# Optimization experiments

Measured on AMD Instinct MI355X. Metric: run time of the kernel, lower is better.

Reference implementation:

```python
import jax, jax.numpy as jnp
import numpy as np

EPS = 1e-5
SLOPE = 0.2


def _conv3d(x, w, stride):
    # x: [B, Cin, D, H, W], w: [Cout, Cin, 3, 3, 3]
    return jax.lax.conv_general_dilated(
        x, w, window_strides=(stride, stride, stride),
        padding=[(1, 1), (1, 1), (1, 1)],
        dimension_numbers=("NCDHW", "OIDHW", "NCDHW"))


def _layernorm_c(y, g, b):
    # LayerNorm over the channel (feature) dim, matching nn.LayerNorm(C) on [N, C]
    mu = jnp.mean(y, axis=1, keepdims=True)
    var = jnp.mean((y - mu) ** 2, axis=1, keepdims=True)
    yn = (y - mu) * jax.lax.rsqrt(var + EPS)
    return yn * g[None, :, None, None, None] + b[None, :, None, None, None]


def _leaky(y):
    return jnp.where(y > 0, y, SLOPE * y)


def _block(x, m, w, g, b, stride):
    # x already zero at inactive sites, so dense conv == sparse gather-scatter conv
    y = _conv3d(x, w, stride)
    if stride > 1:
        # strided SparseConv3d: output active iff any input in 3x3x3 window active
        ones_k = jnp.ones((1, 1, 3, 3, 3), x.dtype)
        m = (_conv3d(m, ones_k, stride) > 0).astype(x.dtype)
    y = _leaky(_layernorm_c(y, g, b))
    return y * m, m


def setup_inputs() -> dict:
    key = jax.random.key(0)
    ks = jax.random.split(key, 16)
    B, D = 2, 64
    x = jax.random.normal(ks[0], (B, 3, D, D, D), jnp.float32)
    mask = jax.random.randint(ks[1], (B, D, D, D), 0, 2) > 0
    chans = [(3, 64), (64, 128), (128, 256), (256, 512)]
    inp = {"x": x, "mask": mask}
    for i, (ci, co) in enumerate(chans):
        inp[f"w{i+1}"] = jax.random.normal(ks[2 + 3 * i], (co, ci, 3, 3, 3), jnp.float32) * 0.05
        inp[f"g{i+1}"] = jnp.ones((co,), jnp.float32)
        inp[f"b{i+1}"] = jnp.zeros((co,), jnp.float32)
    return inp


def reference(x, mask, w1, g1, b1, w2, g2, b2, w3, g3, b3, w4, g4, b4):
    m = mask.astype(x.dtype)[:, None]          # [B,1,D,H,W]
    x = x * m                                  # zero inactive sites
    # SubMConv3d: active set unchanged (stride 1)
    y, m = _block(x, m, w1, g1, b1, 1)
    y, m = _block(y, m, w2, g2, b2, 2)
    y, m = _block(y, m, w3, g3, b3, 2)
    y, m = _block(y, m, w4, g4, b4, 2)
    # .dense() fills inactive sites with 0 (already the case), then amax over D,H,W
    return jnp.max(y, axis=(2, 3, 4))          # [B, 512]
```

## Files before the change

kernel.cpp:

```cpp
#include <hip/hip_runtime.h>
#include <hip/hip_bf16.h>
#include <stdint.h>

#define EPS 1e-5f
#define SLOPE 0.2f

typedef __attribute__((ext_vector_type(8))) short short8;
typedef __attribute__((ext_vector_type(4))) float f32x4;

static __device__ inline ushort f2bf(float f) {
  __hip_bfloat16 h = __float2bfloat16(f);
  return *reinterpret_cast<ushort*>(&h);
}

static __device__ inline short8 u4_to_s8(uint a, uint b, uint c, uint d) {
  union { uint4 u; short8 s; } cv;
  cv.u.x = a; cv.u.y = b; cv.u.z = c; cv.u.w = d;
  return cv.s;
}

__global__ void mask_detect_k(const uint8_t* __restrict__ raw, int nbytes,
                              unsigned* __restrict__ flag) {
  unsigned local = 0;
  for (int i = blockIdx.x * blockDim.x + threadIdx.x; i < nbytes;
       i += gridDim.x * blockDim.x)
    if (i & 3) local |= raw[i];
  if (local) atomicOr(flag, 1u);
}

__global__ void xclm_k(const float* __restrict__ x, const uint8_t* __restrict__ raw,
                       const unsigned* __restrict__ flag,
                       uint8_t* __restrict__ m1, ushort* __restrict__ xcl) {
  int id = blockIdx.x * blockDim.x + threadIdx.x;
  if (id >= 2 * 262144) return;
  uint8_t v;
  if (*flag) {
    v = raw[id];
  } else {
    size_t j = 4 * (size_t)id;
    v = (uint8_t)(raw[j] | raw[j + 1] | raw[j + 2] | raw[j + 3]);
  }
  v = v ? 1 : 0;
  m1[id] = v;
  float mk = (float)v;
  int b  = id >> 18;
  int sp = id & 262143;
  size_t base = (size_t)b * 3 * 262144 + sp;
  float x0 = x[base] * mk;
  float x1 = x[base + 262144] * mk;
  float x2 = x[base + 2 * 262144] * mk;
  uint2 u;
  u.x = ((uint)f2bf(x1) << 16) | (uint)f2bf(x0);
  u.y = (uint)f2bf(x2);
  *reinterpret_cast<uint2*>(xcl + (size_t)id * 4) = u;
}

__global__ void mask_down_k(const uint8_t* __restrict__ mi,
                            uint8_t* __restrict__ mo, int DIN) {
  int W = DIN >> 1;
  int id = blockIdx.x * blockDim.x + threadIdx.x;
  int total = 2 * W * W * W;
  if (id >= total) return;
  int xo = id % W; int t = id / W;
  int yo = t % W;  t /= W;
  int zo = t % W;  int b = t / W;
  int any = 0;
  for (int dz = 0; dz < 3; ++dz) {
    int z = 2 * zo + dz - 1; if (z < 0 || z >= DIN) continue;
    for (int dy = 0; dy < 3; ++dy) {
      int y = 2 * yo + dy - 1; if (y < 0 || y >= DIN) continue;
      for (int dx = 0; dx < 3; ++dx) {
        int x = 2 * xo + dx - 1; if (x < 0 || x >= DIN) continue;
        any |= mi[(((size_t)b * DIN + z) * DIN + y) * DIN + x];
      }
    }
  }
  mo[id] = any ? 1 : 0;
}

__global__ void wprep_k(const float* __restrict__ w1, const float* __restrict__ w2,
                        const float* __restrict__ w3, const float* __restrict__ w4,
                        ushort* __restrict__ wb1, ushort* __restrict__ wb2,
                        ushort* __restrict__ wb3, ushort* __restrict__ wb4) {
  int id = blockIdx.x * blockDim.x + threadIdx.x;
  if (id < 8192) {
    int k = id & 127, c = id >> 7;
    int tap = k >> 2, ci = k & 3;
    float v = (tap < 27 && ci < 3) ? w1[c * 81 + ci * 27 + tap] : 0.f;
    wb1[id] = f2bf(v);
    return;
  }
  id -= 8192;
  if (id < 128 * 1728) {
    int kn = id % 1728, c = id / 1728;
    int off = kn >> 6, ci = kn & 63;
    wb2[(size_t)c * 1728 + kn] = f2bf(w2[(size_t)c * 1728 + ci * 27 + off]);
    return;
  }
  id -= 128 * 1728;
  if (id < 256 * 3456) {
    int kn = id % 3456, c = id / 3456;
    int off = kn >> 7, ci = kn & 127;
    wb3[(size_t)c * 3456 + kn] = f2bf(w3[(size_t)c * 3456 + ci * 27 + off]);
    return;
  }
  id -= 256 * 3456;
  if (id < 512 * 6912) {
    int kn = id % 6912, c = id / 6912;
    int off = kn >> 8, ci = kn & 255;
    wb4[(size_t)c * 6912 + kn] = f2bf(w4[(size_t)c * 6912 + ci * 27 + off]);
  }
}

__global__ __launch_bounds__(256) void conv1_gemm(
    const ushort* __restrict__ xcl,
    const ushort* __restrict__ wb1,
    const float* __restrict__ gamma,
    const float* __restrict__ beta,
    const uint8_t* __restrict__ msk,
    ushort* __restrict__ out,
    const ushort* __restrict__ zpage)
{
  const int t    = threadIdx.x;
  const int lane = t & 63;
  const int wave = t >> 6;
  int bid = blockIdx.x;
  bid = (bid & 7) * 512 + (bid >> 3);
  const int n0 = bid * 128;
  const int wn = wave * 32;

  __shared__ short As[2][64 * 64];
  __shared__ short Bs[2][128 * 64];

  const int nl   = t & 127;
  const int kchi = t >> 7;
  const int ng = n0 + nl;
  const int bx = ng & 63, by = (ng >> 6) & 63, bz = (ng >> 12) & 63;
  const long basevox = (long)ng * 4;
  const bool okx0 = bx > 0, okx2 = bx < 63;
  const bool oky0 = by > 0, oky2 = by < 63;
  const bool okz0 = bz > 0, okz2 = bz < 63;
  int bswz[4];
#pragma unroll
  for (int j = 0; j < 4; ++j) {
    int kc = kchi + 2 * j;
    bswz[j] = nl * 64 + ((kc ^ (nl & 7)) << 3);
  }
  int aswz[2];
  const ushort* aptr[2];
#pragma unroll
  for (int j = 0; j < 2; ++j) {
    int q = t + 256 * j, ml = q >> 3, kc = q & 7;
    aswz[j] = ml * 64 + ((kc ^ (ml & 7)) << 3);
    aptr[j] = wb1 + ml * 128 + kc * 8;
  }

  short8 ar[2], br[4];

  auto LOADK = [&](int kb) {
#pragma unroll
    for (int j = 0; j < 2; ++j)
      ar[j] = *reinterpret_cast<const short8*>(aptr[j] + kb * 64);
#pragma unroll
    for (int j = 0; j < 4; ++j) {
      int tp0 = kb * 16 + (kchi + 2 * j) * 2;
      uint wrd[4];
#pragma unroll
      for (int h = 0; h < 2; ++h) {
        int tp = tp0 + h;
        int dz = tp / 9, rr = tp - dz * 9;
        int dy = rr / 3, dx = rr - dy * 3;
        bool ok = (tp < 27)
               && (dz != 0 || okz0) && (dz != 2 || okz2)
               && (dy != 0 || oky0) && (dy != 2 || oky2)
               && (dx != 0 || okx0) && (dx != 2 || okx2);
        long toff = (long)(((dz - 1) * 4096 + (dy - 1) * 64 + (dx - 1)) * 4);
        const ushort* p = ok ? (xcl + basevox + toff) : zpage;
        uint2 v = *reinterpret_cast<const uint2*>(p);
        wrd[2 * h] = v.x; wrd[2 * h + 1] = v.y;
      }
      br[j] = u4_to_s8(wrd[0], wrd[1], wrd[2], wrd[3]);
    }
  };

  auto WRITEK = [&](int buf) {
#pragma unroll
    for (int j = 0; j < 2; ++j)
      *reinterpret_cast<short8*>(&As[buf][aswz[j]]) = ar[j];
#pragma unroll
    for (int j = 0; j < 4; ++j)
      *reinterpret_cast<short8*>(&Bs[buf][bswz[j]]) = br[j];
  };

  f32x4 acc[4][2];
#pragma unroll
  for (int i = 0; i < 4; ++i)
#pragma unroll
    for (int j = 0; j < 2; ++j) acc[i][j] = (f32x4)(0.f);

  auto COMPUTE = [&](int buf) {
    short8 afr[4][2], bfr[2][2];
#pragma unroll
    for (int mf = 0; mf < 4; ++mf)
#pragma unroll
      for (int kh = 0; kh < 2; ++kh) {
        int row  = mf * 16 + (lane & 15);
        int slot = (lane >> 4) + kh * 4;
        afr[mf][kh] = *reinterpret_cast<const short8*>(
            &As[buf][row * 64 + ((slot ^ (row & 7)) << 3)]);
      }
#pragma unroll
    for (int nf = 0; nf < 2; ++nf)
#pragma unroll
      for (int kh = 0; kh < 2; ++kh) {
        int row  = wn + nf * 16 + (lane & 15);
        int slot = (lane >> 4) + kh * 4;
        bfr[nf][kh] = *reinterpret_cast<const short8*>(
            &Bs[buf][row * 64 + ((slot ^ (row & 7)) << 3)]);
      }
#pragma unroll
    for (int mf = 0; mf < 4; ++mf)
#pragma unroll
      for (int nf = 0; nf < 2; ++nf)
#pragma unroll
        for (int kh = 0; kh < 2; ++kh)
          acc[mf][nf] = __builtin_amdgcn_mfma_f32_16x16x32_bf16(
              afr[mf][kh], bfr[nf][kh], acc[mf][nf], 0, 0, 0);
  };

  LOADK(0);
  WRITEK(0);
  LOADK(1);
  __syncthreads();
  COMPUTE(0);
  WRITEK(1);
  __syncthreads();
  COMPUTE(1);

  float gr[4][4], br_[4][4];
#pragma unroll
  for (int mf = 0; mf < 4; ++mf) {
    int cb = mf * 16 + ((lane >> 4) << 2);
    f32x4 gv = *reinterpret_cast<const f32x4*>(gamma + cb);
    f32x4 bv = *reinterpret_cast<const f32x4*>(beta + cb);
#pragma unroll
    for (int r = 0; r < 4; ++r) { gr[mf][r] = gv[r]; br_[mf][r] = bv[r]; }
  }

#pragma unroll
  for (int nf = 0; nf < 2; ++nf) {
    float s = 0.f, sq = 0.f;
#pragma unroll
    for (int mf = 0; mf < 4; ++mf)
#pragma unroll
      for (int r = 0; r < 4; ++r) {
        float v = acc[mf][nf][r];
        s += v; sq += v * v;
      }
    s  += __shfl_xor(s, 16);  sq += __shfl_xor(sq, 16);
    s  += __shfl_xor(s, 32);  sq += __shfl_xor(sq, 32);
    const float mean = s * (1.f / 64.f);
    const float var  = sq * (1.f / 64.f) - mean * mean;
    const float rstd = rsqrtf(var + EPS);
    const int vox = n0 + wn + nf * 16 + (lane & 15);
    const float mk = msk[vox] ? 1.f : 0.f;
#pragma unroll
    for (int mf = 0; mf < 4; ++mf) {
      uint2 u;
      float r0 = (acc[mf][nf][0] - mean) * rstd * gr[mf][0] + br_[mf][0];
      float r1 = (acc[mf][nf][1] - mean) * rstd * gr[mf][1] + br_[mf][1];
      float r2 = (acc[mf][nf][2] - mean) * rstd * gr[mf][2] + br_[mf][2];
      float r3 = (acc[mf][nf][3] - mean) * rstd * gr[mf][3] + br_[mf][3];
      r0 = (r0 > 0.f ? r0 : SLOPE * r0) * mk;
      r1 = (r1 > 0.f ? r1 : SLOPE * r1) * mk;
      r2 = (r2 > 0.f ? r2 : SLOPE * r2) * mk;
      r3 = (r3 > 0.f ? r3 : SLOPE * r3) * mk;
      u.x = ((uint)f2bf(r1) << 16) | (uint)f2bf(r0);
      u.y = ((uint)f2bf(r3) << 16) | (uint)f2bf(r2);
      *reinterpret_cast<uint2*>(out + (size_t)vox * 64 + mf * 16 +
                                ((lane >> 4) << 2)) = u;
    }
  }
}

__global__ __launch_bounds__(256) void conv2_gemm(
    const ushort* __restrict__ in,
    const ushort* __restrict__ wbf,
    const float* __restrict__ gamma,
    const float* __restrict__ beta,
    const uint8_t* __restrict__ msk,
    ushort* __restrict__ out,
    const ushort* __restrict__ zpage)
{
  constexpr int CIN = 64, DIN = 64, S = 2;
  constexpr int W = 32, K = 1728, NT = 27, LW = 5;

  const int t    = threadIdx.x;
  const int lane = t & 63;
  const int wave = t >> 6;
  int bid = blockIdx.x;
  bid = (bid & 7) * 64 + (bid >> 3);
  const int n0 = bid * 128;

  __shared__ short As[2][128 * 64];
  __shared__ short Bs[2][128 * 64];
  __shared__ float lnS[4][4][16];
  __shared__ float lnQ[4][4][16];

  int zb[4], yb[4], xb[4], kc8[4], swz[4];
  size_t bb[4];
  const ushort* aptr[4];
#pragma unroll
  for (int j = 0; j < 4; ++j) {
    int q  = t + 256 * j;
    int nl = q >> 3, kc = q & 7;
    kc8[j] = kc * 8;
    swz[j] = nl * 64 + ((kc ^ (nl & 7)) << 3);
    int ngv = n0 + nl;
    int xo = ngv & (W - 1), yo = (ngv >> LW) & (W - 1),
        zo = (ngv >> (2 * LW)) & (W - 1), b = ngv >> (3 * LW);
    xb[j] = xo * S; yb[j] = yo * S; zb[j] = zo * S;
    bb[j] = (size_t)b * CIN * DIN * DIN * DIN;
    aptr[j] = wbf + (size_t)nl * K + kc * 8;
  }

  short8 ar[4], br[4];

  auto LOADK = [&](int kb) {
    const int off = kb;
    const int dz = off / 9, rr = off % 9;
    const int dy = rr / 3, dx = rr % 3;
#pragma unroll
    for (int j = 0; j < 4; ++j) {
      ar[j] = *reinterpret_cast<const short8*>(aptr[j] + kb * 64);
      int zin = zb[j] + dz - 1;
      int yin = yb[j] + dy - 1;
      int xin = xb[j] + dx - 1;
      bool ok = ((unsigned)zin < (unsigned)DIN) &&
                ((unsigned)yin < (unsigned)DIN) &&
                ((unsigned)xin < (unsigned)DIN);
      const ushort* p = ok
          ? in + bb[j] + (((size_t)zin * DIN + yin) * DIN + xin) * CIN + kc8[j]
          : zpage;
      br[j] = *reinterpret_cast<const short8*>(p);
    }
  };

  auto WRITEK = [&](int buf) {
#pragma unroll
    for (int j = 0; j < 4; ++j) {
      *reinterpret_cast<short8*>(&As[buf][swz[j]]) = ar[j];
      *reinterpret_cast<short8*>(&Bs[buf][swz[j]]) = br[j];
    }
  };

  f32x4 acc[4][4];
#pragma unroll
  for (int i = 0; i < 4; ++i)
#pragma unroll
    for (int j = 0; j < 4; ++j) acc[i][j] = (f32x4)(0.f);

  const int wm = (wave & 1) * 64;
  const int wn = (wave >> 1) * 64;

  LOADK(0);
  for (int kb = 0; kb < NT; ++kb) {
    const int buf = kb & 1;
    WRITEK(buf);
    if (kb + 1 < NT) LOADK(kb + 1);
    __syncthreads();

    short8 afr[4][2], bfr[4][2];
#pragma unroll
    for (int mf = 0; mf < 4; ++mf)
#pragma unroll
      for (int kh = 0; kh < 2; ++kh) {
        int row  = wm + mf * 16 + (lane & 15);
        int slot = (lane >> 4) + kh * 4;
        afr[mf][kh] = *reinterpret_cast<const short8*>(
            &As[buf][row * 64 + ((slot ^ (row & 7)) << 3)]);
      }
#pragma unroll
    for (int nf = 0; nf < 4; ++nf)
#pragma unroll
      for (int kh = 0; kh < 2; ++kh) {
        int row  = wn + nf * 16 + (lane & 15);
        int slot = (lane >> 4) + kh * 4;
        bfr[nf][kh] = *reinterpret_cast<const short8*>(
            &Bs[buf][row * 64 + ((slot ^ (row & 7)) << 3)]);
      }
#pragma unroll
    for (int mf = 0; mf < 4; ++mf)
#pragma unroll
      for (int nf = 0; nf < 4; ++nf)
#pragma unroll
        for (int kh = 0; kh < 2; ++kh)
          acc[mf][nf] = __builtin_amdgcn_mfma_f32_16x16x32_bf16(
              afr[mf][kh], bfr[nf][kh], acc[mf][nf], 0, 0, 0);
  }

  float sv[4], qv[4];
#pragma unroll
  for (int nf = 0; nf < 4; ++nf) {
    float s = 0.f, sq = 0.f;
#pragma unroll
    for (int mf = 0; mf < 4; ++mf)
#pragma unroll
      for (int r = 0; r < 4; ++r) {
        float v = acc[mf][nf][r];
        s += v; sq += v * v;
      }
    s  += __shfl_xor(s, 16);  sq += __shfl_xor(sq, 16);
    s  += __shfl_xor(s, 32);  sq += __shfl_xor(sq, 32);
    sv[nf] = s; qv[nf] = sq;
  }
  if (lane < 16) {
#pragma unroll
    for (int nf = 0; nf < 4; ++nf) {
      lnS[wave][nf][lane] = sv[nf];
      lnQ[wave][nf][lane] = qv[nf];
    }
  }
  __syncthreads();

  float gr[4][4], br_[4][4];
#pragma unroll
  for (int mf = 0; mf < 4; ++mf) {
    int cb = wm + mf * 16 + ((lane >> 4) << 2);
    f32x4 gv = *reinterpret_cast<const f32x4*>(gamma + cb);
    f32x4 bv = *reinterpret_cast<const f32x4*>(beta + cb);
#pragma unroll
    for (int r = 0; r < 4; ++r) { gr[mf][r] = gv[r]; br_[mf][r] = bv[r]; }
  }

#pragma unroll
  for (int nf = 0; nf < 4; ++nf) {
    const float s  = sv[nf] + lnS[wave ^ 1][nf][lane & 15];
    const float sq = qv[nf] + lnQ[wave ^ 1][nf][lane & 15];
    const float mean = s * (1.f / 128.f);
    const float var  = sq * (1.f / 128.f) - mean * mean;
    const float rstd = rsqrtf(var + EPS);
    const int vox = n0 + wn + nf * 16 + (lane & 15);
    const float mk = msk[vox] ? 1.f : 0.f;
#pragma unroll
    for (int mf = 0; mf < 4; ++mf) {
      uint2 u;
      float r0 = (acc[mf][nf][0] - mean) * rstd * gr[mf][0] + br_[mf][0];
      float r1 = (acc[mf][nf][1] - mean) * rstd * gr[mf][1] + br_[mf][1];
      float r2 = (acc[mf][nf][2] - mean) * rstd * gr[mf][2] + br_[mf][2];
      float r3 = (acc[mf][nf][3] - mean) * rstd * gr[mf][3] + br_[mf][3];
      r0 = (r0 > 0.f ? r0 : SLOPE * r0) * mk;
      r1 = (r1 > 0.f ? r1 : SLOPE * r1) * mk;
      r2 = (r2 > 0.f ? r2 : SLOPE * r2) * mk;
      r3 = (r3 > 0.f ? r3 : SLOPE * r3) * mk;
      u.x = ((uint)f2bf(r1) << 16) | (uint)f2bf(r0);
      u.y = ((uint)f2bf(r3) << 16) | (uint)f2bf(r2);
      *reinterpret_cast<uint2*>(out + (size_t)vox * 128 + wm + mf * 16 +
                                ((lane >> 4) << 2)) = u;
    }
  }
}

template <int CIN, int COUT, int DIN, int S, int L2CIN, int SPLITK>
__global__ __launch_bounds__(256) void conv_gemm(
    const ushort* __restrict__ in,
    const ushort* __restrict__ wbf,
    float* __restrict__ rawout,
    const ushort* __restrict__ zpage)
{
  constexpr int W  = DIN / S;
  constexpr int K  = 27 * CIN;
  constexpr int NT = K / 64;
  constexpr int NTS = NT / SPLITK;
  constexpr int LW = (W == 32) ? 5 : (W == 16) ? 4 : 3;
  constexpr size_t NVOX = (size_t)2 * W * W * W;

  const int t    = threadIdx.x;
  const int lane = t & 63;
  const int wave = t >> 6;
  const int n0   = blockIdx.x * 128;
  const int m0   = blockIdx.y * 128;
  const int kb0  = blockIdx.z * NTS;
  float* rawp = rawout + (size_t)blockIdx.z * NVOX * COUT;

  __shared__ short As[2][128 * 64];
  __shared__ short Bs[2][128 * 64];

  int zb[4], yb[4], xb[4], kc8[4], swz[4];
  size_t bb[4];
  const ushort* aptr[4];
#pragma unroll
  for (int j = 0; j < 4; ++j) {
    int q  = t + 256 * j;
    int nl = q >> 3, kc = q & 7;
    kc8[j] = kc * 8;
    swz[j] = nl * 64 + ((kc ^ (nl & 7)) << 3);
    int ng = n0 + nl;
    int xo = ng & (W - 1), yo = (ng >> LW) & (W - 1),
        zo = (ng >> (2 * LW)) & (W - 1), b = ng >> (3 * LW);
    xb[j] = xo * S; yb[j] = yo * S; zb[j] = zo * S;
    bb[j] = (size_t)b * CIN * DIN * DIN * DIN;
    aptr[j] = wbf + (size_t)(m0 + nl) * K + kc * 8;
  }

  short8 ar[4], br[4];

  auto LOADK = [&](int kb) {
    const int off = (kb * 64) >> L2CIN;
    const int ci0 = (kb * 64) & (CIN - 1);
    const int dz = off / 9, rr = off % 9;
    const int dy = rr / 3, dx = rr % 3;
#pragma unroll
    for (int j = 0; j < 4; ++j) {
      ar[j] = *reinterpret_cast<const short8*>(aptr[j] + kb * 64);
      int zin = zb[j] + dz - 1;
      int yin = yb[j] + dy - 1;
      int xin = xb[j] + dx - 1;
      bool ok = ((unsigned)zin < (unsigned)DIN) &&
                ((unsigned)yin < (unsigned)DIN) &&
                ((unsigned)xin < (unsigned)DIN);
      const ushort* p = ok
          ? in + bb[j] + (((size_t)zin * DIN + yin) * DIN + xin) * CIN + ci0 + kc8[j]
          : zpage;
      br[j] = *reinterpret_cast<const short8*>(p);
    }
  };

  auto WRITEK = [&](int buf) {
#pragma unroll
    for (int j = 0; j < 4; ++j) {
      *reinterpret_cast<short8*>(&As[buf][swz[j]]) = ar[j];
      *reinterpret_cast<short8*>(&Bs[buf][swz[j]]) = br[j];
    }
  };

  f32x4 acc[4][4];
#pragma unroll
  for (int i = 0; i < 4; ++i)
#pragma unroll
    for (int j = 0; j < 4; ++j) acc[i][j] = (f32x4)(0.f);

  const int wm = (wave & 1) * 64;
  const int wn = (wave >> 1) * 64;

  LOADK(kb0);
  for (int kb = kb0; kb < kb0 + NTS; ++kb) {
    const int buf = (kb - kb0) & 1;
    WRITEK(buf);
    if (kb + 1 < kb0 + NTS) LOADK(kb + 1);
    __syncthreads();

    short8 afr[4][2], bfr[4][2];
#pragma unroll
    for (int mf = 0; mf < 4; ++mf)
#pragma unroll
      for (int kh = 0; kh < 2; ++kh) {
        int row  = wm + mf * 16 + (lane & 15);
        int slot = (lane >> 4) + kh * 4;
        afr[mf][kh] = *reinterpret_cast<const short8*>(
            &As[buf][row * 64 + ((slot ^ (row & 7)) << 3)]);
      }
#pragma unroll
    for (int nf = 0; nf < 4; ++nf)
#pragma unroll
      for (int kh = 0; kh < 2; ++kh) {
        int row  = wn + nf * 16 + (lane & 15);
        int slot = (lane >> 4) + kh * 4;
        bfr[nf][kh] = *reinterpret_cast<const short8*>(
            &Bs[buf][row * 64 + ((slot ^ (row & 7)) << 3)]);
      }
#pragma unroll
    for (int mf = 0; mf < 4; ++mf)
#pragma unroll
      for (int nf = 0; nf < 4; ++nf)
#pragma unroll
        for (int kh = 0; kh < 2; ++kh)
          acc[mf][nf] = __builtin_amdgcn_mfma_f32_16x16x32_bf16(
              afr[mf][kh], bfr[nf][kh], acc[mf][nf], 0, 0, 0);
  }

#pragma unroll
  for (int mf = 0; mf < 4; ++mf)
#pragma unroll
    for (int nf = 0; nf < 4; ++nf) {
      int mg = m0 + wm + mf * 16 + ((lane >> 4) << 2);
      int ng = n0 + wn + nf * 16 + (lane & 15);
      *reinterpret_cast<f32x4*>(&rawp[(size_t)ng * COUT + mg]) = acc[mf][nf];
    }
}

template <int C, int NPART, bool BF16OUT>
__global__ __launch_bounds__(256) void ln_mask_k(
    const float* __restrict__ raw,
    const float* __restrict__ gamma,
    const float* __restrict__ beta,
    const uint8_t* __restrict__ msk,
    void* __restrict__ outv, int nvox)
{
  constexpr int E = C / 64;
  const int lane = threadIdx.x & 63;
  const int vox  = blockIdx.x * 4 + (threadIdx.x >> 6);
  if (vox >= nvox) return;

  const size_t stride = (size_t)nvox * C;
  const float* p = raw + (size_t)vox * C;
  float v[E];
  float s = 0.f, sq = 0.f;
#pragma unroll
  for (int e = 0; e < E; ++e) {
    float acc = 0.f;
#pragma unroll
    for (int pt = 0; pt < NPART; ++pt) acc += p[pt * stride + e * 64 + lane];
    v[e] = acc;
    s += acc; sq += acc * acc;
  }
#pragma unroll
  for (int off = 32; off; off >>= 1) {
    s  += __shfl_xor(s, off);
    sq += __shfl_xor(sq, off);
  }
  const float mean = s / (float)C;
  const float var  = sq / (float)C - mean * mean;
  const float rstd = rsqrtf(var + EPS);
  const float mk   = msk[vox] ? 1.f : 0.f;

#pragma unroll
  for (int e = 0; e < E; ++e) {
    int c = e * 64 + lane;
    float r = (v[e] - mean) * rstd * gamma[c] + beta[c];
    r = (r > 0.f ? r : SLOPE * r) * mk;
    if (BF16OUT)
      ((ushort*)outv)[(size_t)vox * C + c] = f2bf(r);
    else
      ((float*)outv)[(size_t)vox * C + c] = r;
  }
}

__global__ __launch_bounds__(256) void ln4max_k(
    const float* __restrict__ raw,
    const float* __restrict__ gamma,
    const float* __restrict__ beta,
    const uint8_t* __restrict__ msk,
    float* __restrict__ pm)
{
  const int t    = threadIdx.x;
  const int lane = t & 63;
  const int wave = t >> 6;
  const int grp  = blockIdx.x;
  const size_t stride = (size_t)1024 * 512;

  float gg[8], bb_[8];
#pragma unroll
  for (int e = 0; e < 8; ++e) {
    int c = e * 64 + lane;
    gg[e] = gamma[c]; bb_[e] = beta[c];
  }

  float vmax[8];
#pragma unroll
  for (int e = 0; e < 8; ++e) vmax[e] = -1e30f;

  for (int it = 0; it < 16; ++it) {
    const int vox = grp * 64 + wave * 16 + it;
    const float* p = raw + (size_t)vox * 512;
    float v[8];
    float s = 0.f, sq = 0.f;
#pragma unroll
    for (int e = 0; e < 8; ++e) {
      float a = 0.f;
#pragma unroll
      for (int pt = 0; pt < 4; ++pt) a += p[pt * stride + e * 64 + lane];
      v[e] = a; s += a; sq += a * a;
    }
#pragma unroll
    for (int off = 32; off; off >>= 1) {
      s  += __shfl_xor(s, off);
      sq += __shfl_xor(sq, off);
    }
    const float mean = s * (1.f / 512.f);
    const float var  = sq * (1.f / 512.f) - mean * mean;
    const float rstd = rsqrtf(var + EPS);
    const float mk   = msk[vox] ? 1.f : 0.f;
#pragma unroll
    for (int e = 0; e < 8; ++e) {
      float r = (v[e] - mean) * rstd * gg[e] + bb_[e];
      r = (r > 0.f ? r : SLOPE * r) * mk;
      vmax[e] = fmaxf(vmax[e], r);
    }
  }

  __shared__ float red[4][512];
#pragma unroll
  for (int e = 0; e < 8; ++e) red[wave][e * 64 + lane] = vmax[e];
  __syncthreads();
  for (int c = t; c < 512; c += 256) {
    float m = fmaxf(fmaxf(red[0][c], red[1][c]), fmaxf(red[2][c], red[3][c]));
    pm[(size_t)grp * 512 + c] = m;
  }
}

__global__ void rmax2_k(const float* __restrict__ pm, float* __restrict__ out) {
  const int b = blockIdx.x;
  const int c = threadIdx.x;
  float m = -1e30f;
  for (int g = 0; g < 8; ++g) m = fmaxf(m, pm[((size_t)b * 8 + g) * 512 + c]);
  out[b * 512 + c] = m;
}

extern "C" void kernel_launch(void* const* d_in, const int* in_sizes, int n_in,
                              void* d_out, int out_size, void* d_ws, size_t ws_size,
                              hipStream_t stream) {
  const float*   x    = (const float*)d_in[0];
  const uint8_t* mraw = (const uint8_t*)d_in[1];
  const float* w1 = (const float*)d_in[2];
  const float* g1 = (const float*)d_in[3];
  const float* b1 = (const float*)d_in[4];
  const float* w2 = (const float*)d_in[5];
  const float* g2 = (const float*)d_in[6];
  const float* b2 = (const float*)d_in[7];
  const float* w3 = (const float*)d_in[8];
  const float* g3 = (const float*)d_in[9];
  const float* b3 = (const float*)d_in[10];
  const float* w4 = (const float*)d_in[11];
  const float* g4 = (const float*)d_in[12];
  const float* b4 = (const float*)d_in[13];
  float* out = (float*)d_out;
  char*  ws  = (char*)d_ws;

  const size_t ZP  = 0;
  const size_t T1  = 256;
  const size_t R3  = 67109120;
  const size_t R4  = R3 + 16777216;
  const size_t T2  = 100663552;
  const size_t T3  = 117440768;
  const size_t PM  = 123732224;
  const size_t XCL = 123764992;
  const size_t WB1 = 127959296;
  const size_t WB2 = 127975680;
  const size_t WB3 = 128418048;
  const size_t WB4 = 130187520;
  const size_t M1  = 137265408;
  const size_t M2  = 137789696;
  const size_t M3  = 137855232;
  const size_t M4  = 137863424;

  unsigned* flag = (unsigned*)(ws + ZP);
  const ushort* zpage = (const ushort*)(ws + ZP + 16);
  ushort* t1  = (ushort*)(ws + T1);
  float*  r3  = (float*)(ws + R3);
  float*  r4  = (float*)(ws + R4);
  ushort* t2  = (ushort*)(ws + T2);
  ushort* t3  = (ushort*)(ws + T3);
  float*  pm  = (float*)(ws + PM);
  ushort* xcl = (ushort*)(ws + XCL);
  ushort* wb1 = (ushort*)(ws + WB1);
  ushort* wb2 = (ushort*)(ws + WB2);
  ushort* wb3 = (ushort*)(ws + WB3);
  ushort* wb4 = (ushort*)(ws + WB4);
  uint8_t* m1 = (uint8_t*)(ws + M1);
  uint8_t* m2 = (uint8_t*)(ws + M2);
  uint8_t* m3 = (uint8_t*)(ws + M3);
  uint8_t* m4 = (uint8_t*)(ws + M4);

  const int NM1 = 2 * 64 * 64 * 64;

  hipMemsetAsync(ws + ZP, 0, 64, stream);
  mask_detect_k<<<256, 256, 0, stream>>>(mraw, NM1, flag);
  xclm_k<<<NM1 / 256, 256, 0, stream>>>(x, mraw, flag, m1, xcl);
  mask_down_k<<<(2 * 32 * 32 * 32 + 255) / 256, 256, 0, stream>>>(m1, m2, 64);
  mask_down_k<<<(2 * 16 * 16 * 16 + 255) / 256, 256, 0, stream>>>(m2, m3, 32);
  mask_down_k<<<(2 * 8 * 8 * 8 + 255) / 256, 256, 0, stream>>>(m3, m4, 16);

  wprep_k<<<18176, 256, 0, stream>>>(w1, w2, w3, w4, wb1, wb2, wb3, wb4);

  conv1_gemm<<<4096, 256, 0, stream>>>(xcl, wb1, g1, b1, m1, t1, zpage);

  conv2_gemm<<<512, 256, 0, stream>>>(t1, wb2, g2, b2, m2, t2, zpage);

  conv_gemm<128, 256, 32, 2, 7, 2><<<dim3(64, 2, 2), 256, 0, stream>>>(t2, wb3, r3, zpage);
  ln_mask_k<256, 2, true><<<8192 / 4, 256, 0, stream>>>(r3, g3, b3, m3, t3, 8192);

  conv_gemm<256, 512, 16, 2, 8, 4><<<dim3(8, 4, 4), 256, 0, stream>>>(t3, wb4, r4, zpage);
  ln4max_k<<<16, 256, 0, stream>>>(r4, g4, b4, m4, pm);

  rmax2_k<<<2, 512, 0, stream>>>(pm, out);

  (void)in_sizes; (void)n_in; (void)out_size; (void)ws_size;
}
```

Before: 203.7 us.

## Pad conv1 input halo and load MFMA fragments directly from global, dropping LDS staging

The first-layer input is written into a zero-padded 66^3 channel-last buffer, so conv1 can gather taps without bounds checks. Conv1 and conv2 no longer stage A and B tiles through shared memory with double buffering and barriers. Each lane loads its MFMA fragments straight from global memory, with boundary taps in conv2 handled by a precomputed bitmask. This removes LDS traffic and __syncthreads, but adds a memset of the padded buffer and more redundant global loads that now rely on cache reuse.

After: 285.7 us. +40.3%, slower.

```diff
diff --git a/kernel.cpp b/kernel.cpp
--- a/kernel.cpp
+++ b/kernel.cpp
@@ -30,7 +30,7 @@
 
 __global__ void xclm_k(const float* __restrict__ x, const uint8_t* __restrict__ raw,
                        const unsigned* __restrict__ flag,
-                       uint8_t* __restrict__ m1, ushort* __restrict__ xcl) {
+                       uint8_t* __restrict__ m1, ushort* __restrict__ xclp) {
   int id = blockIdx.x * blockDim.x + threadIdx.x;
   if (id >= 2 * 262144) return;
   uint8_t v;
@@ -45,6 +45,7 @@
   float mk = (float)v;
   int b  = id >> 18;
   int sp = id & 262143;
+  int xx = sp & 63, yy = (sp >> 6) & 63, zz = sp >> 12;
   size_t base = (size_t)b * 3 * 262144 + sp;
   float x0 = x[base] * mk;
   float x1 = x[base + 262144] * mk;
@@ -52,7 +53,8 @@
   uint2 u;
   u.x = ((uint)f2bf(x1) << 16) | (uint)f2bf(x0);
   u.y = (uint)f2bf(x2);
-  *reinterpret_cast<uint2*>(xcl + (size_t)id * 4) = u;
+  size_t pidx = ((((size_t)(b * 66 + zz + 1)) * 66 + (yy + 1)) * 66 + (xx + 1)) * 4;
+  *reinterpret_cast<uint2*>(xclp + pidx) = u;
 }
 
 __global__ void mask_down_k(const uint8_t* __restrict__ mi,
@@ -113,84 +115,58 @@
 }
 
 __global__ __launch_bounds__(256) void conv1_gemm(
-    const ushort* __restrict__ xcl,
+    const ushort* __restrict__ xclp,
     const ushort* __restrict__ wb1,
     const float* __restrict__ gamma,
     const float* __restrict__ beta,
     const uint8_t* __restrict__ msk,
-    ushort* __restrict__ out,
-    const ushort* __restrict__ zpage)
+    ushort* __restrict__ out)
 {
   const int t    = threadIdx.x;
   const int lane = t & 63;
   const int wave = t >> 6;
+  const int c8   = lane >> 4;
   int bid = blockIdx.x;
   bid = (bid & 7) * 512 + (bid >> 3);
   const int n0 = bid * 128;
   const int wn = wave * 32;
 
-  __shared__ short As[2][64 * 64];
-  __shared__ short Bs[2][128 * 64];
-
-  const int nl   = t & 127;
-  const int kchi = t >> 7;
-  const int ng = n0 + nl;
-  const int bx = ng & 63, by = (ng >> 6) & 63, bz = (ng >> 12) & 63;
-  const long basevox = (long)ng * 4;
-  const bool okx0 = bx > 0, okx2 = bx < 63;
-  const bool oky0 = by > 0, oky2 = by < 63;
-  const bool okz0 = bz > 0, okz2 = bz < 63;
-  int bswz[4];
-#pragma unroll
-  for (int j = 0; j < 4; ++j) {
-    int kc = kchi + 2 * j;
-    bswz[j] = nl * 64 + ((kc ^ (nl & 7)) << 3);
-  }
-  int aswz[2];
-  const ushort* aptr[2];
-#pragma unroll
-  for (int j = 0; j < 2; ++j) {
-    int q = t + 256 * j, ml = q >> 3, kc = q & 7;
-    aswz[j] = ml * 64 + ((kc ^ (ml & 7)) << 3);
-    aptr[j] = wb1 + ml * 128 + kc * 8;
-  }
-
-  short8 ar[2], br[4];
-
-  auto LOADK = [&](int kb) {
-#pragma unroll
-    for (int j = 0; j < 2; ++j)
-      ar[j] = *reinterpret_cast<const short8*>(aptr[j] + kb * 64);
-#pragma unroll
-    for (int j = 0; j < 4; ++j) {
-      int tp0 = kb * 16 + (kchi + 2 * j) * 2;
-      uint wrd[4];
-#pragma unroll
-      for (int h = 0; h < 2; ++h) {
-        int tp = tp0 + h;
-        int dz = tp / 9, rr = tp - dz * 9;
-        int dy = rr / 3, dx = rr - dy * 3;
-        bool ok = (tp < 27)
-               && (dz != 0 || okz0) && (dz != 2 || okz2)
-               && (dy != 0 || oky0) && (dy != 2 || oky2)
-               && (dx != 0 || okx0) && (dx != 2 || okx2);
-        long toff = (long)(((dz - 1) * 4096 + (dy - 1) * 64 + (dx - 1)) * 4);
-        const ushort* p = ok ? (xcl + basevox + toff) : zpage;
-        uint2 v = *reinterpret_cast<const uint2*>(p);
-        wrd[2 * h] = v.x; wrd[2 * h + 1] = v.y;
-      }
-      br[j] = u4_to_s8(wrd[0], wrd[1], wrd[2], wrd[3]);
-    }
-  };
-
-  auto WRITEK = [&](int buf) {
-#pragma unroll
-    for (int j = 0; j < 2; ++j)
-      *reinterpret_cast<short8*>(&As[buf][aswz[j]]) = ar[j];
-#pragma unroll
-    for (int j = 0; j < 4; ++j)
-      *reinterpret_cast<short8*>(&Bs[buf][bswz[j]]) = br[j];
-  };
+  long pbase[2];
+#pragma unroll
+  for (int nf = 0; nf < 2; ++nf) {
+    int vox = n0 + wn + nf * 16 + (lane & 15);
+    int xx = vox & 63, yy = (vox >> 6) & 63, zz = (vox >> 12) & 63, b = vox >> 18;
+    pbase[nf] = ((((long)(b * 66 + zz + 1)) * 66 + (yy + 1)) * 66 + (xx + 1)) * 4;
+  }
+
+  int toff[2][2][2];
+#pragma unroll
+  for (int kb = 0; kb < 2; ++kb)
+#pragma unroll
+    for (int kh = 0; kh < 2; ++kh)
+#pragma unroll
+      for (int p = 0; p < 2; ++p) {
+        int tap = kb * 16 + kh * 8 + c8 * 2 + p;
+        int off = 0;
+        if (tap < 27) {
+          int dz = tap / 9, rr = tap - dz * 9;
+          int dy = rr / 3, dx = rr - dy * 3;
+          off = ((dz - 1) * 66 * 66 + (dy - 1) * 66 + (dx - 1)) * 4;
+        }
+        toff[kb][kh][p] = off;
+      }
+
+  short8 afr[2][4][2];
+#pragma unroll
+  for (int kb = 0; kb < 2; ++kb)
+#pragma unroll
+    for (int mf = 0; mf < 4; ++mf)
+#pragma unroll
+      for (int kh = 0; kh < 2; ++kh) {
+        int row = mf * 16 + (lane & 15);
+        int k   = kb * 64 + (c8 + kh * 4) * 8;
+        afr[kb][mf][kh] = *reinterpret_cast<const short8*>(wb1 + row * 128 + k);
+      }
 
   f32x4 acc[4][2];
 #pragma unroll
@@ -198,44 +174,20 @@
 #pragma unroll
     for (int j = 0; j < 2; ++j) acc[i][j] = (f32x4)(0.f);
 
-  auto COMPUTE = [&](int buf) {
-    short8 afr[4][2], bfr[2][2];
-#pragma unroll
-    for (int mf = 0; mf < 4; ++mf)
+#pragma unroll
+  for (int kb = 0; kb < 2; ++kb)
+#pragma unroll
+    for (int nf = 0; nf < 2; ++nf)
 #pragma unroll
       for (int kh = 0; kh < 2; ++kh) {
-        int row  = mf * 16 + (lane & 15);
-        int slot = (lane >> 4) + kh * 4;
-        afr[mf][kh] = *reinterpret_cast<const short8*>(
-            &As[buf][row * 64 + ((slot ^ (row & 7)) << 3)]);
-      }
-#pragma unroll
-    for (int nf = 0; nf < 2; ++nf)
-#pragma unroll
-      for (int kh = 0; kh < 2; ++kh) {
-        int row  = wn + nf * 16 + (lane & 15);
-        int slot = (lane >> 4) + kh * 4;
-        bfr[nf][kh] = *reinterpret_cast<const short8*>(
-            &Bs[buf][row * 64 + ((slot ^ (row & 7)) << 3)]);
-      }
-#pragma unroll
-    for (int mf = 0; mf < 4; ++mf)
-#pragma unroll
-      for (int nf = 0; nf < 2; ++nf)
-#pragma unroll
-        for (int kh = 0; kh < 2; ++kh)
+        uint2 v0 = *reinterpret_cast<const uint2*>(xclp + pbase[nf] + toff[kb][kh][0]);
+        uint2 v1 = *reinterpret_cast<const uint2*>(xclp + pbase[nf] + toff[kb][kh][1]);
+        short8 bfr = u4_to_s8(v0.x, v0.y, v1.x, v1.y);
+#pragma unroll
+        for (int mf = 0; mf < 4; ++mf)
           acc[mf][nf] = __builtin_amdgcn_mfma_f32_16x16x32_bf16(
-              afr[mf][kh], bfr[nf][kh], acc[mf][nf], 0, 0, 0);
-  };
-
-  LOADK(0);
-  WRITEK(0);
-  LOADK(1);
-  __syncthreads();
-  COMPUTE(0);
-  WRITEK(1);
-  __syncthreads();
-  COMPUTE(1);
+              afr[kb][mf][kh], bfr, acc[mf][nf], 0, 0, 0);
+      }
 
   float gr[4][4], br_[4][4];
 #pragma unroll
@@ -292,67 +244,38 @@
     ushort* __restrict__ out,
     const ushort* __restrict__ zpage)
 {
-  constexpr int CIN = 64, DIN = 64, S = 2;
-  constexpr int W = 32, K = 1728, NT = 27, LW = 5;
-
   const int t    = threadIdx.x;
   const int lane = t & 63;
   const int wave = t >> 6;
+  const int c8   = lane >> 4;
   int bid = blockIdx.x;
   bid = (bid & 7) * 64 + (bid >> 3);
   const int n0 = bid * 128;
-
-  __shared__ short As[2][128 * 64];
-  __shared__ short Bs[2][128 * 64];
+  const int wm = (wave & 1) * 64;
+  const int wn = (wave >> 1) * 64;
+
   __shared__ float lnS[4][4][16];
   __shared__ float lnQ[4][4][16];
 
-  int zb[4], yb[4], xb[4], kc8[4], swz[4];
-  size_t bb[4];
-  const ushort* aptr[4];
-#pragma unroll
-  for (int j = 0; j < 4; ++j) {
-    int q  = t + 256 * j;
-    int nl = q >> 3, kc = q & 7;
-    kc8[j] = kc * 8;
-    swz[j] = nl * 64 + ((kc ^ (nl & 7)) << 3);
-    int ngv = n0 + nl;
-    int xo = ngv & (W - 1), yo = (ngv >> LW) & (W - 1),
-        zo = (ngv >> (2 * LW)) & (W - 1), b = ngv >> (3 * LW);
-    xb[j] = xo * S; yb[j] = yo * S; zb[j] = zo * S;
-    bb[j] = (size_t)b * CIN * DIN * DIN * DIN;
-    aptr[j] = wbf + (size_t)nl * K + kc * 8;
-  }
-
-  short8 ar[4], br[4];
-
-  auto LOADK = [&](int kb) {
-    const int off = kb;
-    const int dz = off / 9, rr = off % 9;
-    const int dy = rr / 3, dx = rr % 3;
-#pragma unroll
-    for (int j = 0; j < 4; ++j) {
-      ar[j] = *reinterpret_cast<const short8*>(aptr[j] + kb * 64);
-      int zin = zb[j] + dz - 1;
-      int yin = yb[j] + dy - 1;
-      int xin = xb[j] + dx - 1;
-      bool ok = ((unsigned)zin < (unsigned)DIN) &&
-                ((unsigned)yin < (unsigned)DIN) &&
-                ((unsigned)xin < (unsigned)DIN);
-      const ushort* p = ok
-          ? in + bb[j] + (((size_t)zin * DIN + yin) * DIN + xin) * CIN + kc8[j]
-          : zpage;
-      br[j] = *reinterpret_cast<const short8*>(p);
-    }
-  };
-
-  auto WRITEK = [&](int buf) {
-#pragma unroll
-    for (int j = 0; j < 4; ++j) {
-      *reinterpret_cast<short8*>(&As[buf][swz[j]]) = ar[j];
-      *reinterpret_cast<short8*>(&Bs[buf][swz[j]]) = br[j];
-    }
-  };
+  const ushort* pv[4];
+  uint vmask[4];
+#pragma unroll
+  for (int nf = 0; nf < 4; ++nf) {
+    int vox = n0 + wn + nf * 16 + (lane & 15);
+    int xx = vox & 31, yy = (vox >> 5) & 31, zz = (vox >> 10) & 31, b = vox >> 15;
+    long vaddr = ((((long)(b * 64 + zz * 2)) * 64 + yy * 2) * 64 + xx * 2) * 64;
+    pv[nf] = in + vaddr + c8 * 8;
+    uint bad = 0;
+    if (zz == 0) bad |= 0x1FFu;
+    if (yy == 0) bad |= 0x1C0E07u;
+    if (xx == 0) bad |= 0x1249249u;
+    vmask[nf] = 0x7FFFFFFu & ~bad;
+  }
+
+  const ushort* pa[4];
+#pragma unroll
+  for (int mf = 0; mf < 4; ++mf)
+    pa[mf] = wbf + (size_t)(wm + mf * 16 + (lane & 15)) * 1728 + c8 * 8;
 
   f32x4 acc[4][4];
 #pragma unroll
@@ -360,35 +283,26 @@
 #pragma unroll
     for (int j = 0; j < 4; ++j) acc[i][j] = (f32x4)(0.f);
 
-  const int wm = (wave & 1) * 64;
-  const int wn = (wave >> 1) * 64;
-
-  LOADK(0);
-  for (int kb = 0; kb < NT; ++kb) {
-    const int buf = kb & 1;
-    WRITEK(buf);
-    if (kb + 1 < NT) LOADK(kb + 1);
-    __syncthreads();
+  for (int kb = 0; kb < 27; ++kb) {
+    const int dz = kb / 9, rr = kb - dz * 9;
+    const int dy = rr / 3, dx = rr - dy * 3;
+    const long tapoff = ((long)(dz - 1) * 4096 + (dy - 1) * 64 + (dx - 1)) * 64;
 
     short8 afr[4][2], bfr[4][2];
 #pragma unroll
     for (int mf = 0; mf < 4; ++mf)
 #pragma unroll
+      for (int kh = 0; kh < 2; ++kh)
+        afr[mf][kh] = *reinterpret_cast<const short8*>(pa[mf] + kb * 64 + kh * 32);
+#pragma unroll
+    for (int nf = 0; nf < 4; ++nf) {
+      const bool ok = (vmask[nf] >> kb) & 1;
+#pragma unroll
       for (int kh = 0; kh < 2; ++kh) {
-        int row  = wm + mf * 16 + (lane & 15);
-        int slot = (lane >> 4) + kh * 4;
-        afr[mf][kh] = *reinterpret_cast<const short8*>(
-            &As[buf][row * 64 + ((slot ^ (row & 7)) << 3)]);
-      }
-#pragma unroll
-    for (int nf = 0; nf < 4; ++nf)
-#pragma unroll
-      for (int kh = 0; kh < 2; ++kh) {
-        int row  = wn + nf * 16 + (lane & 15);
-        int slot = (lane >> 4) + kh * 4;
-        bfr[nf][kh] = *reinterpret_cast<const short8*>(
-            &Bs[buf][row * 64 + ((slot ^ (row & 7)) << 3)]);
-      }
+        const ushort* p = ok ? (pv[nf] + tapoff + kh * 32) : zpage;
+        bfr[nf][kh] = *reinterpret_cast<const short8*>(p);
+      }
+    }
 #pragma unroll
     for (int mf = 0; mf < 4; ++mf)
 #pragma unroll
@@ -727,53 +641,55 @@
   float* out = (float*)d_out;
   char*  ws  = (char*)d_ws;
 
-  const size_t ZP  = 0;
-  const size_t T1  = 256;
-  const size_t R3  = 67109120;
-  const size_t R4  = R3 + 16777216;
-  const size_t T2  = 100663552;
-  const size_t T3  = 117440768;
-  const size_t PM  = 123732224;
-  const size_t XCL = 123764992;
-  const size_t WB1 = 127959296;
-  const size_t WB2 = 127975680;
-  const size_t WB3 = 128418048;
-  const size_t WB4 = 130187520;
-  const size_t M1  = 137265408;
-  const size_t M2  = 137789696;
-  const size_t M3  = 137855232;
-  const size_t M4  = 137863424;
+  const size_t ZP   = 0;
+  const size_t T1   = 256;
+  const size_t R3   = 67109120;
+  const size_t R4   = 83886336;
+  const size_t T2   = 92274944;
+  const size_t T3   = 109052160;
+  const size_t PM   = 113246464;
+  const size_t XCLP = 113279232;
+  const size_t XCLP_BYTES = 4600064;
+  const size_t WB1  = XCLP + XCLP_BYTES;
+  const size_t WB2  = WB1 + 16384;
+  const size_t WB3  = WB2 + 442368;
+  const size_t WB4  = WB3 + 1769472;
+  const size_t M1   = WB4 + 7077888;
+  const size_t M2   = M1 + 524288;
+  const size_t M3   = M2 + 65536;
+  const size_t M4   = M3 + 8192;
 
   unsigned* flag = (unsigned*)(ws + ZP);
   const ushort* zpage = (const ushort*)(ws + ZP + 16);
-  ushort* t1  = (ushort*)(ws + T1);
-  float*  r3  = (float*)(ws + R3);
-  float*  r4  = (float*)(ws + R4);
-  ushort* t2  = (ushort*)(ws + T2);
-  ushort* t3  = (ushort*)(ws + T3);
-  float*  pm  = (float*)(ws + PM);
-  ushort* xcl = (ushort*)(ws + XCL);
-  ushort* wb1 = (ushort*)(ws + WB1);
-  ushort* wb2 = (ushort*)(ws + WB2);
-  ushort* wb3 = (ushort*)(ws + WB3);
-  ushort* wb4 = (ushort*)(ws + WB4);
-  uint8_t* m1 = (uint8_t*)(ws + M1);
-  uint8_t* m2 = (uint8_t*)(ws + M2);
-  uint8_t* m3 = (uint8_t*)(ws + M3);
-  uint8_t* m4 = (uint8_t*)(ws + M4);
+  ushort* t1   = (ushort*)(ws + T1);
+  float*  r3   = (float*)(ws + R3);
+  float*  r4   = (float*)(ws + R4);
+  ushort* t2   = (ushort*)(ws + T2);
+  ushort* t3   = (ushort*)(ws + T3);
+  float*  pm   = (float*)(ws + PM);
+  ushort* xclp = (ushort*)(ws + XCLP);
+  ushort* wb1  = (ushort*)(ws + WB1);
+  ushort* wb2  = (ushort*)(ws + WB2);
+  ushort* wb3  = (ushort*)(ws + WB3);
+  ushort* wb4  = (ushort*)(ws + WB4);
+  uint8_t* m1  = (uint8_t*)(ws + M1);
+  uint8_t* m2  = (uint8_t*)(ws + M2);
+  uint8_t* m3  = (uint8_t*)(ws + M3);
+  uint8_t* m4  = (uint8_t*)(ws + M4);
 
   const int NM1 = 2 * 64 * 64 * 64;
 
   hipMemsetAsync(ws + ZP, 0, 64, stream);
+  hipMemsetAsync(ws + XCLP, 0, XCLP_BYTES, stream);
   mask_detect_k<<<256, 256, 0, stream>>>(mraw, NM1, flag);
-  xclm_k<<<NM1 / 256, 256, 0, stream>>>(x, mraw, flag, m1, xcl);
+  xclm_k<<<NM1 / 256, 256, 0, stream>>>(x, mraw, flag, m1, xclp);
   mask_down_k<<<(2 * 32 * 32 * 32 + 255) / 256, 256, 0, stream>>>(m1, m2, 64);
   mask_down_k<<<(2 * 16 * 16 * 16 + 255) / 256, 256, 0, stream>>>(m2, m3, 32);
   mask_down_k<<<(2 * 8 * 8 * 8 + 255) / 256, 256, 0, stream>>>(m3, m4, 16);
 
   wprep_k<<<18176, 256, 0, stream>>>(w1, w2, w3, w4, wb1, wb2, wb3, wb4);
 
-  conv1_gemm<<<4096, 256, 0, stream>>>(xcl, wb1, g1, b1, m1, t1, zpage);
+  conv1_gemm<<<4096, 256, 0, stream>>>(xclp, wb1, g1, b1, m1, t1);
 
   conv2_gemm<<<512, 256, 0, stream>>>(t1, wb2, g2, b2, m2, t2, zpage);
 
```
